# Performance work log

Hardware: AMD Instinct MI355X
Metric: run time of the kernel (lower is better)

## Reference

```python
import jax, jax.numpy as jnp
import numpy as np

N_HEAD = 16
MASKED_BIAS = -10000.0


def setup_inputs() -> dict:
    key = jax.random.key(0)
    k1, k2, k3 = jax.random.split(key, 3)
    B, T, E = 2, 2048, 1024
    return {
        "stacked": jax.random.normal(k1, (B, T, E), dtype=jnp.float32),
        "w_attn": jax.random.normal(k2, (E, 3 * E), dtype=jnp.float32) * 0.02,
        "b_attn": jnp.zeros((3 * E,), dtype=jnp.float32),
        "w_proj": jax.random.normal(k3, (E, E), dtype=jnp.float32) * 0.02,
        "b_proj": jnp.zeros((E,), dtype=jnp.float32),
    }


def reference(stacked, w_attn, b_attn, w_proj, b_proj):
    B, T, E = stacked.shape
    nh = N_HEAD
    dh = E // nh
    # Conv1D (GPT-2): x @ W + b
    qkv = stacked @ w_attn + b_attn            # (B, T, 3E)
    q, k, v = jnp.split(qkv, 3, axis=-1)
    q = q.reshape(B, T, nh, dh).transpose(0, 2, 1, 3)  # (B, nh, T, dh)
    k = k.reshape(B, T, nh, dh).transpose(0, 2, 1, 3)
    v = v.reshape(B, T, nh, dh).transpose(0, 2, 1, 3)
    # scores = Q @ K^T / sqrt(dh)
    w = jnp.einsum("bhtd,bhsd->bhts", q, k) / jnp.sqrt(jnp.float32(dh))
    causal = jnp.tril(jnp.ones((T, T), dtype=bool))
    w = jnp.where(causal, w, jnp.float32(MASKED_BIAS))
    w = jax.nn.softmax(w, axis=-1)
    out = jnp.einsum("bhts,bhsd->bhtd", w, v)  # (B, nh, T, dh)
    out = out.transpose(0, 2, 1, 3).reshape(B, T, E)
    attn_z = out @ w_proj + b_proj
    return attn_z
```

## Files before the change

### kernel.cpp

```cpp
#include <hip/hip_runtime.h>
#include <hip/hip_bf16.h>

#define B_ 2
#define T_ 2048
#define E_ 1024
#define NH 16
#define M_ (B_*T_)
#define N3E 3072

typedef __attribute__((ext_vector_type(8))) short short8;
typedef __attribute__((ext_vector_type(4))) float f32x4;

__device__ __forceinline__ unsigned short f2bf(float f) {
  unsigned u = __builtin_bit_cast(unsigned, f);
  unsigned r = 0x7FFFu + ((u >> 16) & 1u);
  return (unsigned short)((u + r) >> 16);
}

__device__ __forceinline__ float bf2f(unsigned short s) {
  return __builtin_bit_cast(float, ((unsigned)s) << 16);
}

__device__ __forceinline__ unsigned cvtpk(float a, float b) {
  unsigned r;
  asm("v_cvt_pk_bf16_f32 %0, %1, %2" : "=v"(r) : "v"(a), "v"(b));
  return r;
}

__device__ __forceinline__ float exp2fast(float x) {
  float r;
  asm("v_exp_f32 %0, %1" : "=v"(r) : "v"(x));
  return r;
}

__device__ __forceinline__ void gload16(const void* g, void* l) {
  __builtin_amdgcn_global_load_lds(
      (const __attribute__((address_space(1))) unsigned int*)g,
      (__attribute__((address_space(3))) unsigned int*)l, 16, 0, 0);
}

__global__ void cast_kernel(const float* __restrict__ in,
                            unsigned short* __restrict__ out, int n8) {
  int i = blockIdx.x * blockDim.x + threadIdx.x;
  if (i >= n8) return;
  const float4* p = (const float4*)in + (size_t)i * 2;
  float4 a = p[0], b = p[1];
  short8 o;
  o[0] = (short)f2bf(a.x); o[1] = (short)f2bf(a.y);
  o[2] = (short)f2bf(a.z); o[3] = (short)f2bf(a.w);
  o[4] = (short)f2bf(b.x); o[5] = (short)f2bf(b.y);
  o[6] = (short)f2bf(b.z); o[7] = (short)f2bf(b.w);
  *(short8*)(out + (size_t)i * 8) = o;
}

__global__ void transpose_cast(const float* __restrict__ in,
                               unsigned short* __restrict__ out, int R, int C) {
  __shared__ float tile[32][33];
  int c0 = blockIdx.x * 32, r0 = blockIdx.y * 32;
  int tx = threadIdx.x & 31, ty = threadIdx.x >> 5;
#pragma unroll
  for (int i = 0; i < 4; i++) {
    int r = ty + i * 8;
    tile[r][tx] = in[(size_t)(r0 + r) * C + c0 + tx];
  }
  __syncthreads();
#pragma unroll
  for (int i = 0; i < 4; i++) {
    int r = ty + i * 8;
    out[(size_t)(c0 + r) * R + r0 + tx] = f2bf(tile[tx][r]);
  }
}

__global__ __launch_bounds__(256) void vtrans_kernel(
    const unsigned short* __restrict__ qkv, unsigned short* __restrict__ Vt) {
  const int s0 = blockIdx.x * 64;
  const int c0 = blockIdx.y * 64;
  const int b = blockIdx.z;
  __shared__ unsigned short t[64][72];
  const int tid = threadIdx.x;
  const size_t rs = 3 * E_;
  const unsigned short* src = qkv + (size_t)(b * T_) * rs + 2 * E_;
#pragma unroll
  for (int p = 0; p < 2; p++) {
    int idx = tid + p * 256;
    int r = idx >> 3, c = (idx & 7) * 8;
    *(short8*)&t[r][c] = *(const short8*)(src + (size_t)(s0 + r) * rs + c0 + c);
  }
  __syncthreads();
#pragma unroll
  for (int p = 0; p < 2; p++) {
    int idx = tid + p * 256;
    int dr = idx >> 3, sc = (idx & 7) * 8;
    short8 o;
#pragma unroll
    for (int j = 0; j < 8; j++) o[j] = (short)t[sc + j][dr];
    *(short8*)&Vt[(size_t)(b * E_ + c0 + dr) * T_ + s0 + sc] = o;
  }
}

template <int OUTF32>
__global__ __launch_bounds__(256) void gemm_bt(
    const unsigned short* __restrict__ A, const unsigned short* __restrict__ Bt,
    const float* __restrict__ bias, void* __restrict__ outp,
    int M, int N, int K) {
  __shared__ __attribute__((aligned(16))) unsigned short Asm[128 * 32];
  __shared__ __attribute__((aligned(16))) unsigned short Bsm[128 * 32];
  const int tid = threadIdx.x;
  const int lane = tid & 63;
  const int wid = tid >> 6;
  const int wr = wid >> 1, wc = wid & 1;
  const int li = lane & 15, g = lane >> 4;
  const int bm = blockIdx.y * 128, bn = blockIdx.x * 128;

  f32x4 acc[4][4] = {};

  const int srow = tid >> 2;
  const int scol = (tid & 3) * 8;
  const unsigned short* Ag = A + (size_t)(bm + srow) * K + scol;
  const unsigned short* Bg = Bt + (size_t)(bn + srow) * K + scol;
  char* AsmB = (char*)Asm;
  char* BsmB = (char*)Bsm;
  const int ldsoff = tid * 16;

  for (int k0 = 0; k0 < K; k0 += 32) {
    __syncthreads();
    gload16(Ag + k0, AsmB + ldsoff);
    gload16(Ag + (size_t)64 * K + k0, AsmB + ldsoff + 4096);
    gload16(Bg + k0, BsmB + ldsoff);
    gload16(Bg + (size_t)64 * K + k0, BsmB + ldsoff + 4096);
    __syncthreads();
    short8 af[4], bf[4];
#pragma unroll
    for (int i = 0; i < 4; i++)
      af[i] = *(const short8*)&Asm[(wr * 64 + i * 16 + li) * 32 + g * 8];
#pragma unroll
    for (int j = 0; j < 4; j++)
      bf[j] = *(const short8*)&Bsm[(wc * 64 + j * 16 + li) * 32 + g * 8];
#pragma unroll
    for (int i = 0; i < 4; i++)
#pragma unroll
      for (int j = 0; j < 4; j++)
        acc[i][j] = __builtin_amdgcn_mfma_f32_16x16x32_bf16(af[i], bf[j],
                                                            acc[i][j], 0, 0, 0);
  }

#pragma unroll
  for (int j = 0; j < 4; j++) {
    int col = bn + wc * 64 + j * 16 + li;
    float bs = bias[col];
#pragma unroll
    for (int i = 0; i < 4; i++) {
      int row0 = bm + wr * 64 + i * 16 + g * 4;
#pragma unroll
      for (int r = 0; r < 4; r++) {
        float v = acc[i][j][r] + bs;
        if (OUTF32)
          ((float*)outp)[(size_t)(row0 + r) * N + col] = v;
        else
          ((unsigned short*)outp)[(size_t)(row0 + r) * N + col] = f2bf(v);
      }
    }
  }
}

__device__ __forceinline__ f32x4 mfma16(short8 a, short8 b, f32x4 c) {
  return __builtin_amdgcn_mfma_f32_16x16x32_bf16(a, b, c, 0, 0, 0);
}

__device__ __forceinline__ void attn_tile(
    const unsigned short* Ksm, const unsigned short* Vts,
    unsigned short (*PsmW)[64], short8 qf0, short8 qf1,
    float& m2, float& l2, f32x4* O, int qrel, bool diag, int li, int g) {
  f32x4 S[4];
  __builtin_amdgcn_s_setprio(1);
#pragma unroll
  for (int ct = 0; ct < 4; ct++) {
    int r = ct * 16 + li;
    int sw = r & 7;
    short8 k0f = *(const short8*)&Ksm[r * 64 + ((g ^ sw) << 3)];
    short8 k1f = *(const short8*)&Ksm[r * 64 + (((g + 4) ^ sw) << 3)];
    f32x4 z = {0.f, 0.f, 0.f, 0.f};
    z = mfma16(k0f, qf0, z);
    z = mfma16(k1f, qf1, z);
    S[ct] = z;
  }
  __builtin_amdgcn_s_setprio(0);

  if (diag) {
#pragma unroll
    for (int ct = 0; ct < 4; ct++)
#pragma unroll
      for (int r = 0; r < 4; r++)
        if (ct * 16 + g * 4 + r > qrel) S[ct][r] = -30000.f;
  }

  float tmax = S[0][0];
#pragma unroll
  for (int ct = 0; ct < 4; ct++)
#pragma unroll
    for (int r = 0; r < 4; r++) tmax = fmaxf(tmax, S[ct][r]);
  tmax = fmaxf(tmax, __shfl_xor(tmax, 16));
  tmax = fmaxf(tmax, __shfl_xor(tmax, 32));

  if (__any(tmax > m2 + 11.5f)) {
    float mn = fmaxf(m2, tmax);
    float cs = exp2fast(m2 - mn);
    l2 *= cs;
#pragma unroll
    for (int c2 = 0; c2 < 4; c2++)
#pragma unroll
      for (int r = 0; r < 4; r++) O[c2][r] *= cs;
    m2 = mn;
  }

  float rsum = 0.f;
#pragma unroll
  for (int ct = 0; ct < 4; ct++) {
    float p0 = exp2fast(S[ct][0] - m2);
    float p1 = exp2fast(S[ct][1] - m2);
    float p2 = exp2fast(S[ct][2] - m2);
    float p3 = exp2fast(S[ct][3] - m2);
    rsum += (p0 + p1) + (p2 + p3);
    uint2 pk;
    pk.x = cvtpk(p0, p1);
    pk.y = cvtpk(p2, p3);
    int pc = (2 * ct + (g >> 1)) ^ (li & 7);
    *(uint2*)&PsmW[li][pc * 8 + (g & 1) * 4] = pk;
  }
  rsum += __shfl_xor(rsum, 16);
  rsum += __shfl_xor(rsum, 32);
  l2 += rsum;

  __builtin_amdgcn_s_setprio(1);
#pragma unroll
  for (int kk = 0; kk < 2; kk++) {
    short8 pf = *(const short8*)&PsmW[li][((4 * kk + g) ^ (li & 7)) * 8];
#pragma unroll
    for (int c2 = 0; c2 < 4; c2++) {
      int d = c2 * 16 + li;
      short8 vf = *(const short8*)&Vts[d * 64 + (((kk * 4 + g) ^ (li & 7)) << 3)];
      O[c2] = mfma16(vf, pf, O[c2]);
    }
  }
  __builtin_amdgcn_s_setprio(0);
}

__global__ __launch_bounds__(256) void attn_kernel(
    const unsigned short* __restrict__ qkv, const unsigned short* __restrict__ Vt,
    unsigned short* __restrict__ aout) {
  const int pair = blockIdx.x;
  const int h = blockIdx.y, b = blockIdx.z;
  const int qa = pair, qb = (T_ / 64 - 1) - pair;
  const int tid = threadIdx.x, lane = tid & 63, w = tid >> 6;
  const int li = lane & 15, g = lane >> 4;

  __shared__ __attribute__((aligned(16))) unsigned short Ksm[2][64 * 64];
  __shared__ __attribute__((aligned(16))) unsigned short Vts[2][64 * 64];
  __shared__ __attribute__((aligned(16))) unsigned short Psm[4][16][64];

  const size_t rs = 3 * E_;
  const unsigned short* base = qkv + (size_t)b * T_ * rs + h * 64;
  const unsigned short* Kg = base + E_;
  const unsigned short* Vtg = Vt + (size_t)(b * E_ + h * 64) * T_;

  const float QSC = 0.18033688f;
  short8 qfa0, qfa1, qfb0, qfb1;
  {
    const unsigned short* qrow = base + (size_t)(qa * 64 + w * 16 + li) * rs;
    short8 v0 = *(const short8*)(qrow + g * 8);
    short8 v1 = *(const short8*)(qrow + 32 + g * 8);
    qrow = base + (size_t)(qb * 64 + w * 16 + li) * rs;
    short8 v2 = *(const short8*)(qrow + g * 8);
    short8 v3 = *(const short8*)(qrow + 32 + g * 8);
#pragma unroll
    for (int j = 0; j < 8; j++) {
      qfa0[j] = (short)f2bf(bf2f((unsigned short)v0[j]) * QSC);
      qfa1[j] = (short)f2bf(bf2f((unsigned short)v1[j]) * QSC);
      qfb0[j] = (short)f2bf(bf2f((unsigned short)v2[j]) * QSC);
      qfb1[j] = (short)f2bf(bf2f((unsigned short)v3[j]) * QSC);
    }
  }

  float ma = -1e30f, la = 0.f, mb = -1e30f, lb = 0.f;
  f32x4 Oa[4] = {}, Ob[4] = {};

#pragma unroll
  for (int p = 0; p < 2; p++) {
    int idx = tid + p * 256;
    int r = idx >> 3, ch = idx & 7;
    int sc = (ch ^ (r & 7)) * 8;
    gload16(Kg + (size_t)r * rs + sc, (char*)&Ksm[0][0] + idx * 16);
    gload16(Vtg + (size_t)r * T_ + sc, (char*)&Vts[0][0] + idx * 16);
  }
  asm volatile("s_waitcnt vmcnt(0)" ::: "memory");
  __syncthreads();

  const int nt = qb + 1;
  for (int kv = 0; kv < nt; kv++) {
    const int cur = kv & 1, nxt = cur ^ 1;
    const bool pre = (kv + 1 < nt);
    if (pre) {
      const int s1 = (kv + 1) * 64;
#pragma unroll
      for (int p = 0; p < 2; p++) {
        int idx = tid + p * 256;
        int r = idx >> 3, ch = idx & 7;
        int sc = (ch ^ (r & 7)) * 8;
        gload16(Kg + (size_t)(s1 + r) * rs + sc,
                (char*)&Ksm[nxt][0] + idx * 16);
        gload16(Vtg + (size_t)r * T_ + s1 + sc,
                (char*)&Vts[nxt][0] + idx * 16);
      }
    }

    attn_tile(&Ksm[cur][0], &Vts[cur][0], Psm[w], qfb0, qfb1, mb, lb, Ob,
              qb * 64 + w * 16 + li - kv * 64, kv == qb, li, g);
    if (kv <= qa)
      attn_tile(&Ksm[cur][0], &Vts[cur][0], Psm[w], qfa0, qfa1, ma, la, Oa,
                qa * 64 + w * 16 + li - kv * 64, kv == qa, li, g);

    asm volatile("s_waitcnt vmcnt(0)" ::: "memory");
    __syncthreads();
  }

  const float inva = 1.f / la, invb = 1.f / lb;
  const int rowa = b * T_ + qa * 64 + w * 16 + li;
  const int rowb = b * T_ + qb * 64 + w * 16 + li;
#pragma unroll
  for (int c2 = 0; c2 < 4; c2++) {
    uint2 oa, ob;
    oa.x = cvtpk(Oa[c2][0] * inva, Oa[c2][1] * inva);
    oa.y = cvtpk(Oa[c2][2] * inva, Oa[c2][3] * inva);
    ob.x = cvtpk(Ob[c2][0] * invb, Ob[c2][1] * invb);
    ob.y = cvtpk(Ob[c2][2] * invb, Ob[c2][3] * invb);
    *(uint2*)&aout[(size_t)rowa * E_ + h * 64 + c2 * 16 + g * 4] = oa;
    *(uint2*)&aout[(size_t)rowb * E_ + h * 64 + c2 * 16 + g * 4] = ob;
  }
}

extern "C" void kernel_launch(void* const* d_in, const int* in_sizes, int n_in,
                              void* d_out, int out_size, void* d_ws,
                              size_t ws_size, hipStream_t stream) {
  const float* stacked = (const float*)d_in[0];
  const float* w_attn = (const float*)d_in[1];
  const float* b_attn = (const float*)d_in[2];
  const float* w_proj = (const float*)d_in[3];
  const float* b_proj = (const float*)d_in[4];
  float* out = (float*)d_out;

  unsigned short* Abf = (unsigned short*)d_ws;
  unsigned short* WaT = Abf + (size_t)M_ * E_;
  unsigned short* WpT = WaT + (size_t)N3E * E_;
  unsigned short* qkv = WpT + (size_t)E_ * E_;
  unsigned short* aout = qkv + (size_t)M_ * N3E;
  unsigned short* Vt = aout + (size_t)M_ * E_;

  cast_kernel<<<(M_ * E_ / 8 + 255) / 256, 256, 0, stream>>>(stacked, Abf,
                                                             M_ * E_ / 8);
  transpose_cast<<<dim3(N3E / 32, E_ / 32), 256, 0, stream>>>(w_attn, WaT, E_,
                                                              N3E);
  transpose_cast<<<dim3(E_ / 32, E_ / 32), 256, 0, stream>>>(w_proj, WpT, E_,
                                                             E_);
  gemm_bt<0><<<dim3(N3E / 128, M_ / 128), 256, 0, stream>>>(Abf, WaT, b_attn,
                                                            qkv, M_, N3E, E_);
  vtrans_kernel<<<dim3(T_ / 64, E_ / 64, B_), 256, 0, stream>>>(qkv, Vt);
  attn_kernel<<<dim3(T_ / 128, NH, B_), 256, 0, stream>>>(qkv, Vt, aout);
  gemm_bt<1><<<dim3(E_ / 128, M_ / 128), 256, 0, stream>>>(aout, WpT, b_proj,
                                                           out, M_, E_, E_);
}
```

Baseline: 130.0 us.

## Fuse prep casts into one kernel; widen GEMM K-tile with swizzled LDS and XCD remap

Merges the input cast and the two weight transpose-casts into a single prep kernel, removing two launches. The GEMM K-step grows from 32 to 64 with an XOR-swizzled LDS layout meant to cut bank conflicts and halve barrier count per K. Workgroups are remapped across the 8 XCDs so neighbouring tiles share L2. The cost is larger LDS use per block, which may lower occupancy.

```diff
diff --git a/kernel.cpp b/kernel.cpp
--- a/kernel.cpp
+++ b/kernel.cpp
@@ -39,25 +39,38 @@
       (__attribute__((address_space(3))) unsigned int*)l, 16, 0, 0);
 }
 
-__global__ void cast_kernel(const float* __restrict__ in,
-                            unsigned short* __restrict__ out, int n8) {
-  int i = blockIdx.x * blockDim.x + threadIdx.x;
-  if (i >= n8) return;
-  const float4* p = (const float4*)in + (size_t)i * 2;
-  float4 a = p[0], b = p[1];
-  short8 o;
-  o[0] = (short)f2bf(a.x); o[1] = (short)f2bf(a.y);
-  o[2] = (short)f2bf(a.z); o[3] = (short)f2bf(a.w);
-  o[4] = (short)f2bf(b.x); o[5] = (short)f2bf(b.y);
-  o[6] = (short)f2bf(b.z); o[7] = (short)f2bf(b.w);
-  *(short8*)(out + (size_t)i * 8) = o;
-}
-
-__global__ void transpose_cast(const float* __restrict__ in,
-                               unsigned short* __restrict__ out, int R, int C) {
+__global__ __launch_bounds__(256) void prep_kernel(
+    const float* __restrict__ stacked, const float* __restrict__ w_attn,
+    const float* __restrict__ w_proj, unsigned short* __restrict__ Abf,
+    unsigned short* __restrict__ WaT, unsigned short* __restrict__ WpT) {
   __shared__ float tile[32][33];
-  int c0 = blockIdx.x * 32, r0 = blockIdx.y * 32;
-  int tx = threadIdx.x & 31, ty = threadIdx.x >> 5;
+  const int bx = blockIdx.x;
+  const int tid = threadIdx.x;
+  if (bx < 2048) {
+    int i = bx * 256 + tid;
+    const float4* p = (const float4*)stacked + (size_t)i * 2;
+    float4 a = p[0], b = p[1];
+    short8 o;
+    o[0] = (short)f2bf(a.x); o[1] = (short)f2bf(a.y);
+    o[2] = (short)f2bf(a.z); o[3] = (short)f2bf(a.w);
+    o[4] = (short)f2bf(b.x); o[5] = (short)f2bf(b.y);
+    o[6] = (short)f2bf(b.z); o[7] = (short)f2bf(b.w);
+    *(short8*)(Abf + (size_t)i * 8) = o;
+    return;
+  }
+  const float* in;
+  unsigned short* out;
+  int R, C, c0, r0;
+  if (bx < 5120) {
+    int b = bx - 2048;
+    in = w_attn; out = WaT; R = E_; C = N3E;
+    c0 = (b % 96) * 32; r0 = (b / 96) * 32;
+  } else {
+    int b = bx - 5120;
+    in = w_proj; out = WpT; R = E_; C = E_;
+    c0 = (b % 32) * 32; r0 = (b / 32) * 32;
+  }
+  int tx = tid & 31, ty = tid >> 5;
 #pragma unroll
   for (int i = 0; i < 4; i++) {
     int r = ty + i * 8;
@@ -103,45 +116,54 @@
     const unsigned short* __restrict__ A, const unsigned short* __restrict__ Bt,
     const float* __restrict__ bias, void* __restrict__ outp,
     int M, int N, int K) {
-  __shared__ __attribute__((aligned(16))) unsigned short Asm[128 * 32];
-  __shared__ __attribute__((aligned(16))) unsigned short Bsm[128 * 32];
+  __shared__ __attribute__((aligned(16))) unsigned short Asm[128 * 64];
+  __shared__ __attribute__((aligned(16))) unsigned short Bsm[128 * 64];
   const int tid = threadIdx.x;
   const int lane = tid & 63;
   const int wid = tid >> 6;
   const int wr = wid >> 1, wc = wid & 1;
   const int li = lane & 15, g = lane >> 4;
-  const int bm = blockIdx.y * 128, bn = blockIdx.x * 128;
+
+  const int ntx = N >> 7;
+  const int nwg = (M >> 7) * ntx;
+  const int cpx = nwg >> 3;
+  const int logical = (blockIdx.x & 7) * cpx + (blockIdx.x >> 3);
+  const int bm = (logical / ntx) << 7;
+  const int bn = (logical % ntx) << 7;
 
   f32x4 acc[4][4] = {};
 
-  const int srow = tid >> 2;
-  const int scol = (tid & 3) * 8;
-  const unsigned short* Ag = A + (size_t)(bm + srow) * K + scol;
-  const unsigned short* Bg = Bt + (size_t)(bn + srow) * K + scol;
-  char* AsmB = (char*)Asm;
-  char* BsmB = (char*)Bsm;
-  const int ldsoff = tid * 16;
-
-  for (int k0 = 0; k0 < K; k0 += 32) {
+  for (int k0 = 0; k0 < K; k0 += 64) {
     __syncthreads();
-    gload16(Ag + k0, AsmB + ldsoff);
-    gload16(Ag + (size_t)64 * K + k0, AsmB + ldsoff + 4096);
-    gload16(Bg + k0, BsmB + ldsoff);
-    gload16(Bg + (size_t)64 * K + k0, BsmB + ldsoff + 4096);
+#pragma unroll
+    for (int p = 0; p < 4; p++) {
+      int idx = tid + p * 256;
+      int r = idx >> 3, ch = idx & 7;
+      int sc = (ch ^ (r & 7)) << 3;
+      gload16(A + (size_t)(bm + r) * K + k0 + sc, (char*)Asm + idx * 16);
+      gload16(Bt + (size_t)(bn + r) * K + k0 + sc, (char*)Bsm + idx * 16);
+    }
     __syncthreads();
-    short8 af[4], bf[4];
-#pragma unroll
-    for (int i = 0; i < 4; i++)
-      af[i] = *(const short8*)&Asm[(wr * 64 + i * 16 + li) * 32 + g * 8];
-#pragma unroll
-    for (int j = 0; j < 4; j++)
-      bf[j] = *(const short8*)&Bsm[(wc * 64 + j * 16 + li) * 32 + g * 8];
-#pragma unroll
-    for (int i = 0; i < 4; i++)
-#pragma unroll
-      for (int j = 0; j < 4; j++)
-        acc[i][j] = __builtin_amdgcn_mfma_f32_16x16x32_bf16(af[i], bf[j],
-                                                            acc[i][j], 0, 0, 0);
+#pragma unroll
+    for (int kk = 0; kk < 2; kk++) {
+      short8 af[4], bf[4];
+#pragma unroll
+      for (int i = 0; i < 4; i++) {
+        int R = wr * 64 + i * 16 + li;
+        af[i] = *(const short8*)&Asm[R * 64 + (((kk * 4 + g) ^ (R & 7)) << 3)];
+      }
+#pragma unroll
+      for (int j = 0; j < 4; j++) {
+        int R = wc * 64 + j * 16 + li;
+        bf[j] = *(const short8*)&Bsm[R * 64 + (((kk * 4 + g) ^ (R & 7)) << 3)];
+      }
+#pragma unroll
+      for (int i = 0; i < 4; i++)
+#pragma unroll
+        for (int j = 0; j < 4; j++)
+          acc[i][j] = __builtin_amdgcn_mfma_f32_16x16x32_bf16(
+              af[i], bf[j], acc[i][j], 0, 0, 0);
+    }
   }
 
 #pragma unroll
@@ -355,16 +377,11 @@
   unsigned short* aout = qkv + (size_t)M_ * N3E;
   unsigned short* Vt = aout + (size_t)M_ * E_;
 
-  cast_kernel<<<(M_ * E_ / 8 + 255) / 256, 256, 0, stream>>>(stacked, Abf,
-                                                             M_ * E_ / 8);
-  transpose_cast<<<dim3(N3E / 32, E_ / 32), 256, 0, stream>>>(w_attn, WaT, E_,
-                                                              N3E);
-  transpose_cast<<<dim3(E_ / 32, E_ / 32), 256, 0, stream>>>(w_proj, WpT, E_,
-                                                             E_);
-  gemm_bt<0><<<dim3(N3E / 128, M_ / 128), 256, 0, stream>>>(Abf, WaT, b_attn,
-                                                            qkv, M_, N3E, E_);
+  prep_kernel<<<6144, 256, 0, stream>>>(stacked, w_attn, w_proj, Abf, WaT, WpT);
+  gemm_bt<0><<<(M_ / 128) * (N3E / 128), 256, 0, stream>>>(Abf, WaT, b_attn,
+                                                           qkv, M_, N3E, E_);
   vtrans_kernel<<<dim3(T_ / 64, E_ / 64, B_), 256, 0, stream>>>(qkv, Vt);
   attn_kernel<<<dim3(T_ / 128, NH, B_), 256, 0, stream>>>(qkv, Vt, aout);
-  gemm_bt<1><<<dim3(E_ / 128, M_ / 128), 256, 0, stream>>>(aout, WpT, b_proj,
-                                                           out, M_, E_, E_);
-}
+  gemm_bt<1><<<(M_ / 128) * (E_ / 128), 256, 0, stream>>>(aout, WpT, b_proj,
+                                                          out, M_, E_, E_);
+}
```

Result: faster. 127.3 us (-2.1%).
